# Optimization experiments

Hardware: AMD Instinct MI355X
Metric: run time of the kernel (lower is better)

Reference implementation:

```python
import jax, jax.numpy as jnp
import numpy as np

B, S, D = 4, 4096, 1024

def setup_inputs() -> dict:
    key = jax.random.key(0)
    ks = jax.random.split(key, 7)
    s = 1.0 / np.sqrt(D)
    return {
        "x":   jax.random.normal(ks[0], (B, S, D), dtype=jnp.float32),
        "Wq":  jax.random.uniform(ks[1], (D, D), jnp.float32, -s, s),
        "bq":  jax.random.uniform(ks[2], (D,),   jnp.float32, -s, s),
        "Wk":  jax.random.uniform(ks[3], (D, D), jnp.float32, -s, s),
        "bk":  jax.random.uniform(ks[4], (D,),   jnp.float32, -s, s),
        "Wv":  jax.random.uniform(ks[5], (D, D), jnp.float32, -s, s),
        "bv":  jax.random.uniform(ks[6], (D,),   jnp.float32, -s, s),
    }

def reference(x, Wq, bq, Wk, bk, Wv, bv):
    # Linear projections (torch Linear: x @ W.T + b; here W stored as [in, out])
    Q = jnp.einsum('bsd,df->bsf', x, Wq) + bq
    K = jnp.einsum('bsd,df->bsf', x, Wk) + bk
    V = jnp.einsum('bsd,df->bsf', x, Wv) + bv
    scale = 1.0 / jnp.sqrt(jnp.asarray(D, dtype=jnp.float32))
    scores = jnp.einsum('bqd,bkd->bqk', Q, K) * scale  # [B, S, S]
    attn = jax.nn.softmax(scores, axis=-1)
    return jnp.einsum('bqk,bkd->bqd', attn, V)
```

## Files before the change

kernel.cpp:

```cpp
#include <hip/hip_runtime.h>
#include <hip/hip_bf16.h>
#include <stdint.h>


typedef __attribute__((ext_vector_type(8))) short bf16x8;
typedef __attribute__((ext_vector_type(4))) float f32x4;

static __device__ __forceinline__ unsigned short f2b(float f) {
  union { float f; unsigned u; } x; x.f = f;
  unsigned u = x.u;
  u += 0x7fffu + ((u >> 16) & 1u);
  return (unsigned short)(u >> 16);
}
static __device__ __forceinline__ float b2f(unsigned short s) {
  union { unsigned u; float f; } x; x.u = ((unsigned)s) << 16;
  return x.f;
}

static __device__ __forceinline__ void gl_lds16(const void* g, void* l) {
  __builtin_amdgcn_global_load_lds(
      (const __attribute__((address_space(1))) void*)(uintptr_t)(g),
      (__attribute__((address_space(3))) void*)(uint32_t)(uintptr_t)(l),
      16, 0, 0);
}

__global__ void convert_x(const float* __restrict__ in,
                          unsigned short* __restrict__ out, int n8) {
  int i = blockIdx.x * blockDim.x + threadIdx.x;
  if (i >= n8) return;
  const float4* p = (const float4*)in + (size_t)i * 2;
  float4 a = p[0], b = p[1];
  bf16x8 o;
  o[0] = (short)f2b(a.x); o[1] = (short)f2b(a.y);
  o[2] = (short)f2b(a.z); o[3] = (short)f2b(a.w);
  o[4] = (short)f2b(b.x); o[5] = (short)f2b(b.y);
  o[6] = (short)f2b(b.z); o[7] = (short)f2b(b.w);
  ((bf16x8*)out)[i] = o;
}

__global__ void transpose_w(const float* __restrict__ in,
                            unsigned short* __restrict__ out) {
  __shared__ float tile[32][33];
  const int tx = threadIdx.x;
  const int x = blockIdx.x * 32 + tx;
  const int y0 = blockIdx.y * 32;
  for (int j = threadIdx.y; j < 32; j += 8)
    tile[j][tx] = in[(size_t)(y0 + j) * 1024 + x];
  __syncthreads();
  const int ox = blockIdx.y * 32 + tx;
  const int oy0 = blockIdx.x * 32;
  for (int j = threadIdx.y; j < 32; j += 8)
    out[(size_t)(oy0 + j) * 1024 + ox] = f2b(tile[tx][j]);
}

template <int OUTF>
__global__ __launch_bounds__(512, 2)
void gemm256(const unsigned short* __restrict__ A, long lda, long sAz,
             const unsigned short* __restrict__ B, long ldb, long sBz,
             void* __restrict__ Cv, long ldc, long sCz,
             const float* __restrict__ bias, int bias_mode,
             int K, float alpha) {
  __shared__ __align__(16) unsigned short As[2][256 * 64];
  __shared__ __align__(16) unsigned short Bs[2][256 * 64];

  const unsigned gx = gridDim.x, gy = gridDim.y;
  const unsigned nwg = gx * gy * gridDim.z;
  const unsigned hwid = (blockIdx.z * gy + blockIdx.y) * gx + blockIdx.x;
  unsigned tile = hwid;
  if ((nwg & 7u) == 0u) tile = (hwid & 7u) * (nwg >> 3) + (hwid >> 3);
  const unsigned bxi = tile % gx;
  const unsigned byi = (tile / gx) % gy;
  const unsigned bzi = tile / (gx * gy);

  const int t = threadIdx.x;
  const int wid = t >> 6, lane = t & 63;
  const int wm = wid >> 2, wn = wid & 3;
  const int fr = lane & 15, fq = lane >> 4;
  const long bm = (long)byi * 256;
  const long bn = (long)bxi * 256;
  const unsigned short* Ab = A + (size_t)bzi * sAz;
  const unsigned short* Bb = B + (size_t)bzi * sBz;

  const int sr = t >> 3;
  const int scol = 8 * ((t & 7) ^ (sr & 7));
  const unsigned short* Ag = Ab + (bm + sr) * lda + scol;
  const unsigned short* Bg = Bb + (bn + sr) * ldb + scol;
  const int ldsw = wid * 512;

  const int NT = K >> 6;
  f32x4 acc[8][4] = {};

#define STAGE(XS, Xg, ld, kt, h, bidx)                                        \
  do {                                                                        \
    gl_lds16(Xg + (size_t)((h) * 128) * (ld) + (size_t)(kt) * 64,             \
             &XS[bidx][(h) * 128 * 64 + ldsw]);                               \
    gl_lds16(Xg + (size_t)((h) * 128 + 64) * (ld) + (size_t)(kt) * 64,        \
             &XS[bidx][((h) * 128 + 64) * 64 + ldsw]);                        \
  } while (0)

  auto rdA = [&](int bidx, int i, int kh) {
    int row = wm * 128 + i * 16 + fr;
    int inb = (kh * 64 + fq * 16) ^ ((fr & 7) << 4);
    return *(const bf16x8*)((const char*)&As[bidx][0] + row * 128 + inb);
  };
  auto rdB = [&](int bidx, int j, int kh) {
    int row = wn * 64 + j * 16 + fr;
    int inb = (kh * 64 + fq * 16) ^ ((fr & 7) << 4);
    return *(const bf16x8*)((const char*)&Bs[bidx][0] + row * 128 + inb);
  };

  STAGE(As, Ag, lda, 0, 0, 0); STAGE(As, Ag, lda, 0, 1, 0);
  STAGE(Bs, Bg, ldb, 0, 0, 0); STAGE(Bs, Bg, ldb, 0, 1, 0);
  asm volatile("s_waitcnt vmcnt(0)" ::: "memory");
  asm volatile("s_barrier" ::: "memory");

  for (int tt = 0; tt < NT; ++tt) {
    const int bidx = tt & 1;
    const int nb = (tt + 1) & 1;
    bf16x8 bfr[4][2], ar[2][2], arn[2][2];

#pragma unroll
    for (int j = 0; j < 4; ++j) {
      bfr[j][0] = rdB(bidx, j, 0);
      bfr[j][1] = rdB(bidx, j, 1);
    }
#pragma unroll
    for (int ii = 0; ii < 2; ++ii) {
      ar[ii][0] = rdA(bidx, ii, 0);
      ar[ii][1] = rdA(bidx, ii, 1);
    }

    if (tt + 1 < NT) {
      STAGE(As, Ag, lda, tt + 1, 0, nb); STAGE(As, Ag, lda, tt + 1, 1, nb);
      STAGE(Bs, Bg, ldb, tt + 1, 0, nb); STAGE(Bs, Bg, ldb, tt + 1, 1, nb);
    }

    __builtin_amdgcn_s_setprio(1);
#pragma unroll
    for (int p = 0; p < 4; ++p) {
      if (p < 3) {
#pragma unroll
        for (int ii = 0; ii < 2; ++ii) {
          arn[ii][0] = rdA(bidx, (p + 1) * 2 + ii, 0);
          arn[ii][1] = rdA(bidx, (p + 1) * 2 + ii, 1);
        }
      }
#pragma unroll
      for (int ii = 0; ii < 2; ++ii)
#pragma unroll
        for (int j = 0; j < 4; ++j) {
          acc[p * 2 + ii][j] = __builtin_amdgcn_mfma_f32_16x16x32_bf16(
              ar[ii][0], bfr[j][0], acc[p * 2 + ii][j], 0, 0, 0);
          acc[p * 2 + ii][j] = __builtin_amdgcn_mfma_f32_16x16x32_bf16(
              ar[ii][1], bfr[j][1], acc[p * 2 + ii][j], 0, 0, 0);
        }
      if (p < 3) {
#pragma unroll
        for (int ii = 0; ii < 2; ++ii) {
          ar[ii][0] = arn[ii][0];
          ar[ii][1] = arn[ii][1];
        }
      }
    }
    __builtin_amdgcn_s_setprio(0);

    asm volatile("s_waitcnt vmcnt(0)" ::: "memory");
    asm volatile("s_barrier" ::: "memory");
  }
#undef STAGE

  char* Cb = (char*)Cv + (size_t)bzi * sCz * (OUTF ? 4 : 2);
  const long crow0 = bm + wm * 128 + fq * 4;
  const long ccol0 = bn + wn * 64 + fr;
#pragma unroll
  for (int i = 0; i < 8; ++i) {
#pragma unroll
    for (int j = 0; j < 4; ++j) {
      const long col = ccol0 + j * 16;
      float badd_c = (bias_mode == 1) ? bias[col] : 0.0f;
#pragma unroll
      for (int r = 0; r < 4; ++r) {
        const long row = crow0 + i * 16 + r;
        float v = acc[i][j][r] * alpha + badd_c;
        if (bias_mode == 2) v += bias[row];
        if (OUTF)
          ((float*)Cb)[row * ldc + col] = v;
        else
          ((unsigned short*)Cb)[row * ldc + col] = f2b(v);
      }
    }
  }
}

__global__ __launch_bounds__(256)
void softmax_rows(unsigned short* __restrict__ S) {
  const int t = threadIdx.x;
  unsigned short* row = S + (size_t)blockIdx.x * 4096;
  const bf16x8* p = (const bf16x8*)row;
  bf16x8 u0 = p[t * 2], u1 = p[t * 2 + 1];

  float v[16];
  float m = -1e30f;
#pragma unroll
  for (int j = 0; j < 8; j++) { v[j] = b2f((unsigned short)u0[j]); }
#pragma unroll
  for (int j = 0; j < 8; j++) { v[8 + j] = b2f((unsigned short)u1[j]); }
#pragma unroll
  for (int j = 0; j < 16; j++) m = fmaxf(m, v[j]);

#pragma unroll
  for (int off = 32; off > 0; off >>= 1) m = fmaxf(m, __shfl_xor(m, off));
  __shared__ float redm[4];
  if ((t & 63) == 0) redm[t >> 6] = m;
  __syncthreads();
  m = fmaxf(fmaxf(redm[0], redm[1]), fmaxf(redm[2], redm[3]));

  float s = 0.0f;
#pragma unroll
  for (int j = 0; j < 16; j++) { v[j] = __expf(v[j] - m); s += v[j]; }
#pragma unroll
  for (int off = 32; off > 0; off >>= 1) s += __shfl_xor(s, off);
  __shared__ float reds[4];
  if ((t & 63) == 0) reds[t >> 6] = s;
  __syncthreads();
  s = reds[0] + reds[1] + reds[2] + reds[3];
  const float inv = 1.0f / s;

  bf16x8 o0, o1;
#pragma unroll
  for (int j = 0; j < 8; j++) o0[j] = (short)f2b(v[j] * inv);
#pragma unroll
  for (int j = 0; j < 8; j++) o1[j] = (short)f2b(v[8 + j] * inv);
  bf16x8* q = (bf16x8*)row;
  q[t * 2] = o0;
  q[t * 2 + 1] = o1;
}

extern "C" void kernel_launch(void* const* d_in, const int* in_sizes, int n_in,
                              void* d_out, int out_size, void* d_ws,
                              size_t ws_size, hipStream_t stream) {
  const float* x  = (const float*)d_in[0];
  const float* Wq = (const float*)d_in[1];
  const float* bq = (const float*)d_in[2];
  const float* Wk = (const float*)d_in[3];
  const float* bk = (const float*)d_in[4];
  const float* Wv = (const float*)d_in[5];
  const float* bv = (const float*)d_in[6];
  float* out = (float*)d_out;

  const int Bb = 4, S = 4096, D = 1024;
  const long BS = (long)Bb * S;
  const size_t MiB = 1u << 20;

  char* base = (char*)d_ws;
  unsigned short* Wqt = (unsigned short*)(base);
  unsigned short* Wkt = (unsigned short*)(base + 2 * MiB);
  unsigned short* Wvt = (unsigned short*)(base + 4 * MiB);
  unsigned short* Qb  = (unsigned short*)(base + 6 * MiB);
  unsigned short* Kb  = (unsigned short*)(base + 38 * MiB);
  unsigned short* Vt  = (unsigned short*)(base + 70 * MiB);
  unsigned short* xb  = (unsigned short*)(base + 102 * MiB);
  unsigned short* Sb  = xb;
  const bool batched = ws_size >= (size_t)(102 + 128) * MiB;

  const int n8 = (int)(BS * D / 8);
  convert_x<<<n8 / 256, 256, 0, stream>>>(x, xb, n8);

  dim3 tb(32, 8), tg(32, 32);
  transpose_w<<<tg, tb, 0, stream>>>(Wq, Wqt);
  transpose_w<<<tg, tb, 0, stream>>>(Wk, Wkt);
  transpose_w<<<tg, tb, 0, stream>>>(Wv, Wvt);

  gemm256<0><<<dim3(D / 256, BS / 256, 1), 512, 0, stream>>>(
      xb, D, 0, Wqt, D, 0, Qb, D, 0, bq, 1, D, 1.0f);
  gemm256<0><<<dim3(D / 256, BS / 256, 1), 512, 0, stream>>>(
      xb, D, 0, Wkt, D, 0, Kb, D, 0, bk, 1, D, 1.0f);
  gemm256<0><<<dim3(BS / 256, D / 256, 1), 512, 0, stream>>>(
      Wvt, D, 0, xb, D, 0, Vt, BS, 0, bv, 2, D, 1.0f);

  const float scale = 0.03125f;
  if (batched) {
    gemm256<0><<<dim3(S / 256, S / 256, Bb), 512, 0, stream>>>(
        Qb, D, (long)S * D, Kb, D, (long)S * D, Sb, S, (long)S * S,
        nullptr, 0, D, scale);
    softmax_rows<<<Bb * S, 256, 0, stream>>>(Sb);
    gemm256<1><<<dim3(D / 256, S / 256, Bb), 512, 0, stream>>>(
        Sb, S, (long)S * S, Vt, BS, (long)S, out, D, (long)S * D,
        nullptr, 0, S, 1.0f);
  } else {
    for (int b = 0; b < Bb; b++) {
      const unsigned short* Qp = Qb + (long)b * S * D;
      const unsigned short* Kp = Kb + (long)b * S * D;
      gemm256<0><<<dim3(S / 256, S / 256, 1), 512, 0, stream>>>(
          Qp, D, 0, Kp, D, 0, Sb, S, 0, nullptr, 0, D, scale);
      softmax_rows<<<S, 256, 0, stream>>>(Sb);
      gemm256<1><<<dim3(D / 256, S / 256, 1), 512, 0, stream>>>(
          Sb, S, 0, Vt + (long)b * S, BS, 0, out + (long)b * S * D, D, 0,
          nullptr, 0, S, 1.0f);
    }
  }
}
```

Measured before the change: 463.9 us.

## Split GEMM K-tile into two half-phases with finer-grained async staging

Reorganizes shared-memory tiles into per-K-half sub-buffers (32 columns each) with a new XOR swizzle. The main loop now runs two phases per 64-wide K tile, each issuing that half's next-tile loads before its MFMAs and waiting only on partial vmcnt. This lets loads and compute interleave at a finer granularity instead of waiting on all loads at the end of each tile. The cost is an extra barrier per tile and more complex vmcnt bookkeeping, where a miscount could cause a race.

```diff
diff --git a/kernel.cpp b/kernel.cpp
--- a/kernel.cpp
+++ b/kernel.cpp
@@ -60,8 +60,8 @@
              void* __restrict__ Cv, long ldc, long sCz,
              const float* __restrict__ bias, int bias_mode,
              int K, float alpha) {
-  __shared__ __align__(16) unsigned short As[2][256 * 64];
-  __shared__ __align__(16) unsigned short Bs[2][256 * 64];
+  __shared__ __align__(16) unsigned short As[2][2][8192];
+  __shared__ __align__(16) unsigned short Bs[2][2][8192];
 
   const unsigned gx = gridDim.x, gy = gridDim.y;
   const unsigned nwg = gx * gy * gridDim.z;
@@ -81,93 +81,80 @@
   const unsigned short* Ab = A + (size_t)bzi * sAz;
   const unsigned short* Bb = B + (size_t)bzi * sBz;
 
-  const int sr = t >> 3;
-  const int scol = 8 * ((t & 7) ^ (sr & 7));
-  const unsigned short* Ag = Ab + (bm + sr) * lda + scol;
-  const unsigned short* Bg = Bb + (bn + sr) * ldb + scol;
-  const int ldsw = wid * 512;
+  const int srow = t >> 2;
+  const int soct8 = (((t & 3) ^ ((t >> 3) & 3))) * 8;
+  const unsigned short* AgS = Ab + (bm + srow) * lda + soct8;
+  const unsigned short* BgS = Bb + (bn + srow) * ldb + soct8;
+  const int dstw = wid * 512;
+  const int rs16 = (fq ^ ((fr >> 1) & 3)) << 4;
 
   const int NT = K >> 6;
   f32x4 acc[8][4] = {};
 
-#define STAGE(XS, Xg, ld, kt, h, bidx)                                        \
+  auto stg = [&](const unsigned short* GS, long ld, unsigned short* region,
+                 int kt, int kh) {
+    const unsigned short* s0 = GS + (size_t)kt * 64 + kh * 32;
+    gl_lds16(s0, region + dstw);
+    gl_lds16(s0 + (size_t)128 * ld, region + 4096 + dstw);
+  };
+  auto rdA = [&](int buf, int kh, int i) {
+    return *(const bf16x8*)((const char*)&As[buf][kh][0] +
+                            (wm * 128 + i * 16 + fr) * 64 + rs16);
+  };
+  auto rdB = [&](int buf, int kh, int j) {
+    return *(const bf16x8*)((const char*)&Bs[buf][kh][0] +
+                            (wn * 64 + j * 16 + fr) * 64 + rs16);
+  };
+
+  stg(AgS, lda, &As[0][0][0], 0, 0); stg(BgS, ldb, &Bs[0][0][0], 0, 0);
+  stg(AgS, lda, &As[0][1][0], 0, 1); stg(BgS, ldb, &Bs[0][1][0], 0, 1);
+  asm volatile("s_waitcnt vmcnt(4)" ::: "memory");
+  asm volatile("s_barrier" ::: "memory");
+
+#define PHASE(kh)                                                             \
   do {                                                                        \
-    gl_lds16(Xg + (size_t)((h) * 128) * (ld) + (size_t)(kt) * 64,             \
-             &XS[bidx][(h) * 128 * 64 + ldsw]);                               \
-    gl_lds16(Xg + (size_t)((h) * 128 + 64) * (ld) + (size_t)(kt) * 64,        \
-             &XS[bidx][((h) * 128 + 64) * 64 + ldsw]);                        \
+    if (tt + 1 < NT) {                                                        \
+      stg(AgS, lda, &As[nb][kh][0], tt + 1, kh);                              \
+      stg(BgS, ldb, &Bs[nb][kh][0], tt + 1, kh);                              \
+    }                                                                         \
+    bf16x8 bfr[4], ar[2], arn[2];                                             \
+    _Pragma("unroll")                                                         \
+    for (int j = 0; j < 4; ++j) bfr[j] = rdB(cb, kh, j);                      \
+    ar[0] = rdA(cb, kh, 0); ar[1] = rdA(cb, kh, 1);                           \
+    __builtin_amdgcn_s_setprio(1);                                            \
+    _Pragma("unroll")                                                         \
+    for (int p = 0; p < 4; ++p) {                                             \
+      if (p < 3) {                                                            \
+        arn[0] = rdA(cb, kh, p * 2 + 2);                                      \
+        arn[1] = rdA(cb, kh, p * 2 + 3);                                      \
+      }                                                                       \
+      _Pragma("unroll")                                                       \
+      for (int ii = 0; ii < 2; ++ii)                                          \
+        _Pragma("unroll")                                                     \
+        for (int j = 0; j < 4; ++j)                                           \
+          acc[p * 2 + ii][j] = __builtin_amdgcn_mfma_f32_16x16x32_bf16(       \
+              ar[ii], bfr[j], acc[p * 2 + ii][j], 0, 0, 0);                   \
+      if (p < 3) { ar[0] = arn[0]; ar[1] = arn[1]; }                          \
+    }                                                                         \
+    __builtin_amdgcn_s_setprio(0);                                            \
   } while (0)
 
-  auto rdA = [&](int bidx, int i, int kh) {
-    int row = wm * 128 + i * 16 + fr;
-    int inb = (kh * 64 + fq * 16) ^ ((fr & 7) << 4);
-    return *(const bf16x8*)((const char*)&As[bidx][0] + row * 128 + inb);
-  };
-  auto rdB = [&](int bidx, int j, int kh) {
-    int row = wn * 64 + j * 16 + fr;
-    int inb = (kh * 64 + fq * 16) ^ ((fr & 7) << 4);
-    return *(const bf16x8*)((const char*)&Bs[bidx][0] + row * 128 + inb);
-  };
-
-  STAGE(As, Ag, lda, 0, 0, 0); STAGE(As, Ag, lda, 0, 1, 0);
-  STAGE(Bs, Bg, ldb, 0, 0, 0); STAGE(Bs, Bg, ldb, 0, 1, 0);
-  asm volatile("s_waitcnt vmcnt(0)" ::: "memory");
-  asm volatile("s_barrier" ::: "memory");
-
   for (int tt = 0; tt < NT; ++tt) {
-    const int bidx = tt & 1;
-    const int nb = (tt + 1) & 1;
-    bf16x8 bfr[4][2], ar[2][2], arn[2][2];
-
-#pragma unroll
-    for (int j = 0; j < 4; ++j) {
-      bfr[j][0] = rdB(bidx, j, 0);
-      bfr[j][1] = rdB(bidx, j, 1);
-    }
-#pragma unroll
-    for (int ii = 0; ii < 2; ++ii) {
-      ar[ii][0] = rdA(bidx, ii, 0);
-      ar[ii][1] = rdA(bidx, ii, 1);
-    }
-
+    const int cb = tt & 1, nb = (tt + 1) & 1;
+    if (tt > 0) {
+      asm volatile("s_waitcnt vmcnt(4)" ::: "memory");
+      asm volatile("s_barrier" ::: "memory");
+    }
+    PHASE(0);
     if (tt + 1 < NT) {
-      STAGE(As, Ag, lda, tt + 1, 0, nb); STAGE(As, Ag, lda, tt + 1, 1, nb);
-      STAGE(Bs, Bg, ldb, tt + 1, 0, nb); STAGE(Bs, Bg, ldb, tt + 1, 1, nb);
-    }
-
-    __builtin_amdgcn_s_setprio(1);
-#pragma unroll
-    for (int p = 0; p < 4; ++p) {
-      if (p < 3) {
-#pragma unroll
-        for (int ii = 0; ii < 2; ++ii) {
-          arn[ii][0] = rdA(bidx, (p + 1) * 2 + ii, 0);
-          arn[ii][1] = rdA(bidx, (p + 1) * 2 + ii, 1);
-        }
-      }
-#pragma unroll
-      for (int ii = 0; ii < 2; ++ii)
-#pragma unroll
-        for (int j = 0; j < 4; ++j) {
-          acc[p * 2 + ii][j] = __builtin_amdgcn_mfma_f32_16x16x32_bf16(
-              ar[ii][0], bfr[j][0], acc[p * 2 + ii][j], 0, 0, 0);
-          acc[p * 2 + ii][j] = __builtin_amdgcn_mfma_f32_16x16x32_bf16(
-              ar[ii][1], bfr[j][1], acc[p * 2 + ii][j], 0, 0, 0);
-        }
-      if (p < 3) {
-#pragma unroll
-        for (int ii = 0; ii < 2; ++ii) {
-          ar[ii][0] = arn[ii][0];
-          ar[ii][1] = arn[ii][1];
-        }
-      }
-    }
-    __builtin_amdgcn_s_setprio(0);
-
-    asm volatile("s_waitcnt vmcnt(0)" ::: "memory");
+      asm volatile("s_waitcnt vmcnt(4)" ::: "memory");
+    } else {
+      asm volatile("s_waitcnt vmcnt(0)" ::: "memory");
+    }
     asm volatile("s_barrier" ::: "memory");
+    PHASE(1);
   }
-#undef STAGE
+#undef PHASE
 
   char* Cb = (char*)Cv + (size_t)bzi * sCz * (OUTF ? 4 : 2);
   const long crow0 = bm + wm * 128 + fq * 4;
```

Measured after the change: 483.5 us. 4.2% more time.

## Switch GEMM to 32x32x16 MFMA with 4 waves per 256x256 tile

Applied to the files above, without the earlier changes.

The GEMM kernel moves from 8 waves issuing 16x16x32 bf16 MFMAs to 4 waves (256 threads) each computing a 128x128 sub-tile with 32x32x16 MFMAs. Each wave reuses more of its LDS fragments per load, so fewer LDS reads are needed per FLOP. The global-to-LDS prefetch of the next tile is now issued before the current tile's fragments are read. In exchange, each lane holds 256 accumulator floats, which raises register pressure. With only 4 waves per block and dropped occupancy hints, there is less latency hiding, and the epilogue store pattern changes.

```diff
diff --git a/kernel.cpp b/kernel.cpp
--- a/kernel.cpp
+++ b/kernel.cpp
@@ -4,7 +4,7 @@
 
 
 typedef __attribute__((ext_vector_type(8))) short bf16x8;
-typedef __attribute__((ext_vector_type(4))) float f32x4;
+typedef __attribute__((ext_vector_type(16))) float f32x16;
 
 static __device__ __forceinline__ unsigned short f2b(float f) {
   union { float f; unsigned u; } x; x.f = f;
@@ -54,7 +54,7 @@
 }
 
 template <int OUTF>
-__global__ __launch_bounds__(512, 2)
+__global__ __launch_bounds__(256)
 void gemm256(const unsigned short* __restrict__ A, long lda, long sAz,
              const unsigned short* __restrict__ B, long ldb, long sBz,
              void* __restrict__ Cv, long ldc, long sCz,
@@ -74,92 +74,77 @@
 
   const int t = threadIdx.x;
   const int wid = t >> 6, lane = t & 63;
-  const int wm = wid >> 2, wn = wid & 3;
-  const int fr = lane & 15, fq = lane >> 4;
+  const int wm = wid >> 1, wn = wid & 1;
+  const int fr = lane & 31;
+  const int fh = lane >> 5;
   const long bm = (long)byi * 256;
   const long bn = (long)bxi * 256;
   const unsigned short* Ab = A + (size_t)bzi * sAz;
   const unsigned short* Bb = B + (size_t)bzi * sBz;
 
-  const int sr = t >> 3;
-  const int scol = 8 * ((t & 7) ^ (sr & 7));
-  const unsigned short* Ag = Ab + (bm + sr) * lda + scol;
-  const unsigned short* Bg = Bb + (bn + sr) * ldb + scol;
-  const int ldsw = wid * 512;
+  const int srow = t >> 3;
+  const int scol = 8 * ((t & 7) ^ ((t >> 3) & 7));
+  const unsigned short* AgS = Ab + (bm + srow) * lda + scol;
+  const unsigned short* BgS = Bb + (bn + srow) * ldb + scol;
+  const int dstw = wid * 512;
 
   const int NT = K >> 6;
-  f32x4 acc[8][4] = {};
-
-#define STAGE(XS, Xg, ld, kt, h, bidx)                                        \
-  do {                                                                        \
-    gl_lds16(Xg + (size_t)((h) * 128) * (ld) + (size_t)(kt) * 64,             \
-             &XS[bidx][(h) * 128 * 64 + ldsw]);                               \
-    gl_lds16(Xg + (size_t)((h) * 128 + 64) * (ld) + (size_t)(kt) * 64,        \
-             &XS[bidx][((h) * 128 + 64) * 64 + ldsw]);                        \
-  } while (0)
-
-  auto rdA = [&](int bidx, int i, int kh) {
-    int row = wm * 128 + i * 16 + fr;
-    int inb = (kh * 64 + fq * 16) ^ ((fr & 7) << 4);
-    return *(const bf16x8*)((const char*)&As[bidx][0] + row * 128 + inb);
+  f32x16 acc[4][4] = {};
+
+  auto stage_tile = [&](int kt, int buf) {
+#pragma unroll
+    for (int h = 0; h < 8; ++h)
+      gl_lds16(AgS + (size_t)(h * 32) * lda + (size_t)kt * 64,
+               &As[buf][h * 2048 + dstw]);
+#pragma unroll
+    for (int h = 0; h < 8; ++h)
+      gl_lds16(BgS + (size_t)(h * 32) * ldb + (size_t)kt * 64,
+               &Bs[buf][h * 2048 + dstw]);
   };
-  auto rdB = [&](int bidx, int j, int kh) {
-    int row = wn * 64 + j * 16 + fr;
-    int inb = (kh * 64 + fq * 16) ^ ((fr & 7) << 4);
-    return *(const bf16x8*)((const char*)&Bs[bidx][0] + row * 128 + inb);
+
+  auto rdA = [&](int buf, int i, int ks) {
+    const int row = wm * 128 + i * 32 + fr;
+    const int sl = ((ks * 2 + fh) ^ (row & 7)) << 4;
+    return *(const bf16x8*)((const char*)&As[buf][0] + row * 128 + sl);
   };
-
-  STAGE(As, Ag, lda, 0, 0, 0); STAGE(As, Ag, lda, 0, 1, 0);
-  STAGE(Bs, Bg, ldb, 0, 0, 0); STAGE(Bs, Bg, ldb, 0, 1, 0);
+  auto rdB = [&](int buf, int j, int ks) {
+    const int row = wn * 128 + j * 32 + fr;
+    const int sl = ((ks * 2 + fh) ^ (row & 7)) << 4;
+    return *(const bf16x8*)((const char*)&Bs[buf][0] + row * 128 + sl);
+  };
+
+  stage_tile(0, 0);
   asm volatile("s_waitcnt vmcnt(0)" ::: "memory");
   asm volatile("s_barrier" ::: "memory");
 
   for (int tt = 0; tt < NT; ++tt) {
-    const int bidx = tt & 1;
-    const int nb = (tt + 1) & 1;
-    bf16x8 bfr[4][2], ar[2][2], arn[2][2];
-
-#pragma unroll
-    for (int j = 0; j < 4; ++j) {
-      bfr[j][0] = rdB(bidx, j, 0);
-      bfr[j][1] = rdB(bidx, j, 1);
-    }
-#pragma unroll
-    for (int ii = 0; ii < 2; ++ii) {
-      ar[ii][0] = rdA(bidx, ii, 0);
-      ar[ii][1] = rdA(bidx, ii, 1);
-    }
-
-    if (tt + 1 < NT) {
-      STAGE(As, Ag, lda, tt + 1, 0, nb); STAGE(As, Ag, lda, tt + 1, 1, nb);
-      STAGE(Bs, Bg, ldb, tt + 1, 0, nb); STAGE(Bs, Bg, ldb, tt + 1, 1, nb);
-    }
+    const int cb = tt & 1, nb = (tt + 1) & 1;
+    if (tt + 1 < NT) stage_tile(tt + 1, nb);
+
+    bf16x8 a[4], b[4], an[4], bn[4];
+#pragma unroll
+    for (int i = 0; i < 4; ++i) a[i] = rdA(cb, i, 0);
+#pragma unroll
+    for (int j = 0; j < 4; ++j) b[j] = rdB(cb, j, 0);
 
     __builtin_amdgcn_s_setprio(1);
 #pragma unroll
-    for (int p = 0; p < 4; ++p) {
-      if (p < 3) {
-#pragma unroll
-        for (int ii = 0; ii < 2; ++ii) {
-          arn[ii][0] = rdA(bidx, (p + 1) * 2 + ii, 0);
-          arn[ii][1] = rdA(bidx, (p + 1) * 2 + ii, 1);
-        }
+    for (int ks = 0; ks < 4; ++ks) {
+      if (ks < 3) {
+#pragma unroll
+        for (int i = 0; i < 4; ++i) an[i] = rdA(cb, i, ks + 1);
+#pragma unroll
+        for (int j = 0; j < 4; ++j) bn[j] = rdB(cb, j, ks + 1);
       }
 #pragma unroll
-      for (int ii = 0; ii < 2; ++ii)
-#pragma unroll
-        for (int j = 0; j < 4; ++j) {
-          acc[p * 2 + ii][j] = __builtin_amdgcn_mfma_f32_16x16x32_bf16(
-              ar[ii][0], bfr[j][0], acc[p * 2 + ii][j], 0, 0, 0);
-          acc[p * 2 + ii][j] = __builtin_amdgcn_mfma_f32_16x16x32_bf16(
-              ar[ii][1], bfr[j][1], acc[p * 2 + ii][j], 0, 0, 0);
-        }
-      if (p < 3) {
-#pragma unroll
-        for (int ii = 0; ii < 2; ++ii) {
-          ar[ii][0] = arn[ii][0];
-          ar[ii][1] = arn[ii][1];
-        }
+      for (int i = 0; i < 4; ++i)
+#pragma unroll
+        for (int j = 0; j < 4; ++j)
+          acc[i][j] = __builtin_amdgcn_mfma_f32_32x32x16_bf16(
+              a[i], b[j], acc[i][j], 0, 0, 0);
+      if (ks < 3) {
+#pragma unroll
+        for (int i = 0; i < 4; ++i) { a[i] = an[i]; b[i] = bn[i]; }
       }
     }
     __builtin_amdgcn_s_setprio(0);
@@ -167,20 +152,19 @@
     asm volatile("s_waitcnt vmcnt(0)" ::: "memory");
     asm volatile("s_barrier" ::: "memory");
   }
-#undef STAGE
 
   char* Cb = (char*)Cv + (size_t)bzi * sCz * (OUTF ? 4 : 2);
-  const long crow0 = bm + wm * 128 + fq * 4;
-  const long ccol0 = bn + wn * 64 + fr;
-#pragma unroll
-  for (int i = 0; i < 8; ++i) {
+  const long crow0 = bm + wm * 128;
+  const long ccol0 = bn + wn * 128;
+#pragma unroll
+  for (int i = 0; i < 4; ++i) {
 #pragma unroll
     for (int j = 0; j < 4; ++j) {
-      const long col = ccol0 + j * 16;
+      const long col = ccol0 + j * 32 + fr;
       float badd_c = (bias_mode == 1) ? bias[col] : 0.0f;
 #pragma unroll
-      for (int r = 0; r < 4; ++r) {
-        const long row = crow0 + i * 16 + r;
+      for (int r = 0; r < 16; ++r) {
+        const long row = crow0 + i * 32 + (r & 3) + 8 * (r >> 2) + 4 * fh;
         float v = acc[i][j][r] * alpha + badd_c;
         if (bias_mode == 2) v += bias[row];
         if (OUTF)
@@ -271,30 +255,30 @@
   transpose_w<<<tg, tb, 0, stream>>>(Wk, Wkt);
   transpose_w<<<tg, tb, 0, stream>>>(Wv, Wvt);
 
-  gemm256<0><<<dim3(D / 256, BS / 256, 1), 512, 0, stream>>>(
+  gemm256<0><<<dim3(D / 256, BS / 256, 1), 256, 0, stream>>>(
       xb, D, 0, Wqt, D, 0, Qb, D, 0, bq, 1, D, 1.0f);
-  gemm256<0><<<dim3(D / 256, BS / 256, 1), 512, 0, stream>>>(
+  gemm256<0><<<dim3(D / 256, BS / 256, 1), 256, 0, stream>>>(
       xb, D, 0, Wkt, D, 0, Kb, D, 0, bk, 1, D, 1.0f);
-  gemm256<0><<<dim3(BS / 256, D / 256, 1), 512, 0, stream>>>(
+  gemm256<0><<<dim3(BS / 256, D / 256, 1), 256, 0, stream>>>(
       Wvt, D, 0, xb, D, 0, Vt, BS, 0, bv, 2, D, 1.0f);
 
   const float scale = 0.03125f;
   if (batched) {
-    gemm256<0><<<dim3(S / 256, S / 256, Bb), 512, 0, stream>>>(
+    gemm256<0><<<dim3(S / 256, S / 256, Bb), 256, 0, stream>>>(
         Qb, D, (long)S * D, Kb, D, (long)S * D, Sb, S, (long)S * S,
         nullptr, 0, D, scale);
     softmax_rows<<<Bb * S, 256, 0, stream>>>(Sb);
-    gemm256<1><<<dim3(D / 256, S / 256, Bb), 512, 0, stream>>>(
+    gemm256<1><<<dim3(D / 256, S / 256, Bb), 256, 0, stream>>>(
         Sb, S, (long)S * S, Vt, BS, (long)S, out, D, (long)S * D,
         nullptr, 0, S, 1.0f);
   } else {
     for (int b = 0; b < Bb; b++) {
       const unsigned short* Qp = Qb + (long)b * S * D;
       const unsigned short* Kp = Kb + (long)b * S * D;
-      gemm256<0><<<dim3(S / 256, S / 256, 1), 512, 0, stream>>>(
+      gemm256<0><<<dim3(S / 256, S / 256, 1), 256, 0, stream>>>(
           Qp, D, 0, Kp, D, 0, Sb, S, 0, nullptr, 0, D, scale);
       softmax_rows<<<S, 256, 0, stream>>>(Sb);
-      gemm256<1><<<dim3(D / 256, S / 256, 1), 512, 0, stream>>>(
+      gemm256<1><<<dim3(D / 256, S / 256, 1), 256, 0, stream>>>(
           Sb, S, 0, Vt + (long)b * S, BS, 0, out + (long)b * S * D, D, 0,
           nullptr, 0, S, 1.0f);
     }
```

After: 532.8 us. 1.15x slower.

## Shrink GEMM tiles to 128x128 and fuse Q/K projections into one GEMM

Applied to the files above, without the earlier changes.

The 256x256, 512-thread GEMM is replaced by a 128x128, 256-thread variant with four waves that each compute a 64x64 sub-tile. Wq and Wk are transposed into one concatenated weight so that Q and K come from a single GEMM writing an interleaved [BS, 2048] buffer, with the bias chosen per column by a split index. The smaller tiles are meant to give more workgroups and better occupancy and wave balance on the GPU. The cost is less data reuse per tile, so more global and LDS traffic per FLOP.

```diff
diff --git a/kernel.cpp b/kernel.cpp
--- a/kernel.cpp
+++ b/kernel.cpp
@@ -54,14 +54,14 @@
 }
 
 template <int OUTF>
-__global__ __launch_bounds__(512, 2)
-void gemm256(const unsigned short* __restrict__ A, long lda, long sAz,
+__global__ __launch_bounds__(256, 2)
+void gemm128(const unsigned short* __restrict__ A, long lda, long sAz,
              const unsigned short* __restrict__ B, long ldb, long sBz,
              void* __restrict__ Cv, long ldc, long sCz,
-             const float* __restrict__ bias, int bias_mode,
-             int K, float alpha) {
-  __shared__ __align__(16) unsigned short As[2][256 * 64];
-  __shared__ __align__(16) unsigned short Bs[2][256 * 64];
+             const float* __restrict__ ba, const float* __restrict__ bb,
+             int nsplit, int bias_mode, int K, float alpha) {
+  __shared__ __align__(16) unsigned short As[2][128 * 64];
+  __shared__ __align__(16) unsigned short Bs[2][128 * 64];
 
   const unsigned gx = gridDim.x, gy = gridDim.y;
   const unsigned nwg = gx * gy * gridDim.z;
@@ -74,75 +74,73 @@
 
   const int t = threadIdx.x;
   const int wid = t >> 6, lane = t & 63;
-  const int wm = wid >> 2, wn = wid & 3;
+  const int wm = wid >> 1, wn = wid & 1;
   const int fr = lane & 15, fq = lane >> 4;
-  const long bm = (long)byi * 256;
-  const long bn = (long)bxi * 256;
+  const long bm = (long)byi * 128;
+  const long bn = (long)bxi * 128;
   const unsigned short* Ab = A + (size_t)bzi * sAz;
   const unsigned short* Bb = B + (size_t)bzi * sBz;
 
   const int sr = t >> 3;
   const int scol = 8 * ((t & 7) ^ (sr & 7));
-  const unsigned short* Ag = Ab + (bm + sr) * lda + scol;
-  const unsigned short* Bg = Bb + (bn + sr) * ldb + scol;
+  const unsigned short* AgS = Ab + (bm + sr) * lda + scol;
+  const unsigned short* BgS = Bb + (bn + sr) * ldb + scol;
   const int ldsw = wid * 512;
 
   const int NT = K >> 6;
-  f32x4 acc[8][4] = {};
-
-#define STAGE(XS, Xg, ld, kt, h, bidx)                                        \
-  do {                                                                        \
-    gl_lds16(Xg + (size_t)((h) * 128) * (ld) + (size_t)(kt) * 64,             \
-             &XS[bidx][(h) * 128 * 64 + ldsw]);                               \
-    gl_lds16(Xg + (size_t)((h) * 128 + 64) * (ld) + (size_t)(kt) * 64,        \
-             &XS[bidx][((h) * 128 + 64) * 64 + ldsw]);                        \
-  } while (0)
-
-  auto rdA = [&](int bidx, int i, int kh) {
-    int row = wm * 128 + i * 16 + fr;
-    int inb = (kh * 64 + fq * 16) ^ ((fr & 7) << 4);
-    return *(const bf16x8*)((const char*)&As[bidx][0] + row * 128 + inb);
+  f32x4 acc[4][4] = {};
+
+  auto stage_tile = [&](int kt, int buf) {
+#pragma unroll
+    for (int h = 0; h < 4; ++h)
+      gl_lds16(AgS + (size_t)(h * 32) * lda + (size_t)kt * 64,
+               &As[buf][h * 2048 + ldsw]);
+#pragma unroll
+    for (int h = 0; h < 4; ++h)
+      gl_lds16(BgS + (size_t)(h * 32) * ldb + (size_t)kt * 64,
+               &Bs[buf][h * 2048 + ldsw]);
   };
-  auto rdB = [&](int bidx, int j, int kh) {
-    int row = wn * 64 + j * 16 + fr;
-    int inb = (kh * 64 + fq * 16) ^ ((fr & 7) << 4);
-    return *(const bf16x8*)((const char*)&Bs[bidx][0] + row * 128 + inb);
+
+  auto rdA = [&](int buf, int m, int kh) {
+    const int row = wm * 64 + m * 16 + fr;
+    const int inb = (kh * 64 + fq * 16) ^ ((fr & 7) << 4);
+    return *(const bf16x8*)((const char*)&As[buf][0] + row * 128 + inb);
   };
-
-  STAGE(As, Ag, lda, 0, 0, 0); STAGE(As, Ag, lda, 0, 1, 0);
-  STAGE(Bs, Bg, ldb, 0, 0, 0); STAGE(Bs, Bg, ldb, 0, 1, 0);
+  auto rdB = [&](int buf, int j, int kh) {
+    const int row = wn * 64 + j * 16 + fr;
+    const int inb = (kh * 64 + fq * 16) ^ ((fr & 7) << 4);
+    return *(const bf16x8*)((const char*)&Bs[buf][0] + row * 128 + inb);
+  };
+
+  stage_tile(0, 0);
   asm volatile("s_waitcnt vmcnt(0)" ::: "memory");
   asm volatile("s_barrier" ::: "memory");
 
   for (int tt = 0; tt < NT; ++tt) {
-    const int bidx = tt & 1;
-    const int nb = (tt + 1) & 1;
+    const int cb = tt & 1, nb = (tt + 1) & 1;
     bf16x8 bfr[4][2], ar[2][2], arn[2][2];
 
 #pragma unroll
     for (int j = 0; j < 4; ++j) {
-      bfr[j][0] = rdB(bidx, j, 0);
-      bfr[j][1] = rdB(bidx, j, 1);
+      bfr[j][0] = rdB(cb, j, 0);
+      bfr[j][1] = rdB(cb, j, 1);
     }
 #pragma unroll
     for (int ii = 0; ii < 2; ++ii) {
-      ar[ii][0] = rdA(bidx, ii, 0);
-      ar[ii][1] = rdA(bidx, ii, 1);
-    }
-
-    if (tt + 1 < NT) {
-      STAGE(As, Ag, lda, tt + 1, 0, nb); STAGE(As, Ag, lda, tt + 1, 1, nb);
-      STAGE(Bs, Bg, ldb, tt + 1, 0, nb); STAGE(Bs, Bg, ldb, tt + 1, 1, nb);
-    }
+      ar[ii][0] = rdA(cb, ii, 0);
+      ar[ii][1] = rdA(cb, ii, 1);
+    }
+
+    if (tt + 1 < NT) stage_tile(tt + 1, nb);
 
     __builtin_amdgcn_s_setprio(1);
 #pragma unroll
-    for (int p = 0; p < 4; ++p) {
-      if (p < 3) {
+    for (int p = 0; p < 2; ++p) {
+      if (p < 1) {
 #pragma unroll
         for (int ii = 0; ii < 2; ++ii) {
-          arn[ii][0] = rdA(bidx, (p + 1) * 2 + ii, 0);
-          arn[ii][1] = rdA(bidx, (p + 1) * 2 + ii, 1);
+          arn[ii][0] = rdA(cb, 2 + ii, 0);
+          arn[ii][1] = rdA(cb, 2 + ii, 1);
         }
       }
 #pragma unroll
@@ -154,7 +152,7 @@
           acc[p * 2 + ii][j] = __builtin_amdgcn_mfma_f32_16x16x32_bf16(
               ar[ii][1], bfr[j][1], acc[p * 2 + ii][j], 0, 0, 0);
         }
-      if (p < 3) {
+      if (p < 1) {
 #pragma unroll
         for (int ii = 0; ii < 2; ++ii) {
           ar[ii][0] = arn[ii][0];
@@ -167,22 +165,23 @@
     asm volatile("s_waitcnt vmcnt(0)" ::: "memory");
     asm volatile("s_barrier" ::: "memory");
   }
-#undef STAGE
 
   char* Cb = (char*)Cv + (size_t)bzi * sCz * (OUTF ? 4 : 2);
-  const long crow0 = bm + wm * 128 + fq * 4;
+  const long crow0 = bm + wm * 64 + fq * 4;
   const long ccol0 = bn + wn * 64 + fr;
 #pragma unroll
-  for (int i = 0; i < 8; ++i) {
+  for (int i = 0; i < 4; ++i) {
 #pragma unroll
     for (int j = 0; j < 4; ++j) {
       const long col = ccol0 + j * 16;
-      float badd_c = (bias_mode == 1) ? bias[col] : 0.0f;
+      float badd_c = 0.0f;
+      if (bias_mode == 1)
+        badd_c = (col < nsplit) ? ba[col] : bb[col - nsplit];
 #pragma unroll
       for (int r = 0; r < 4; ++r) {
         const long row = crow0 + i * 16 + r;
         float v = acc[i][j][r] * alpha + badd_c;
-        if (bias_mode == 2) v += bias[row];
+        if (bias_mode == 2) v += ba[row];
         if (OUTF)
           ((float*)Cb)[row * ldc + col] = v;
         else
@@ -253,50 +252,47 @@
   const size_t MiB = 1u << 20;
 
   char* base = (char*)d_ws;
-  unsigned short* Wqt = (unsigned short*)(base);
-  unsigned short* Wkt = (unsigned short*)(base + 2 * MiB);
-  unsigned short* Wvt = (unsigned short*)(base + 4 * MiB);
-  unsigned short* Qb  = (unsigned short*)(base + 6 * MiB);
-  unsigned short* Kb  = (unsigned short*)(base + 38 * MiB);
-  unsigned short* Vt  = (unsigned short*)(base + 70 * MiB);
-  unsigned short* xb  = (unsigned short*)(base + 102 * MiB);
-  unsigned short* Sb  = xb;
+  unsigned short* Wqkt = (unsigned short*)(base);
+  unsigned short* Wvt  = (unsigned short*)(base + 4 * MiB);
+  unsigned short* QK   = (unsigned short*)(base + 6 * MiB);
+  unsigned short* Vt   = (unsigned short*)(base + 70 * MiB);
+  unsigned short* xb   = (unsigned short*)(base + 102 * MiB);
+  unsigned short* Sb   = xb;
   const bool batched = ws_size >= (size_t)(102 + 128) * MiB;
 
   const int n8 = (int)(BS * D / 8);
   convert_x<<<n8 / 256, 256, 0, stream>>>(x, xb, n8);
 
   dim3 tb(32, 8), tg(32, 32);
-  transpose_w<<<tg, tb, 0, stream>>>(Wq, Wqt);
-  transpose_w<<<tg, tb, 0, stream>>>(Wk, Wkt);
+  transpose_w<<<tg, tb, 0, stream>>>(Wq, Wqkt);
+  transpose_w<<<tg, tb, 0, stream>>>(Wk, Wqkt + (size_t)D * D);
   transpose_w<<<tg, tb, 0, stream>>>(Wv, Wvt);
 
-  gemm256<0><<<dim3(D / 256, BS / 256, 1), 512, 0, stream>>>(
-      xb, D, 0, Wqt, D, 0, Qb, D, 0, bq, 1, D, 1.0f);
-  gemm256<0><<<dim3(D / 256, BS / 256, 1), 512, 0, stream>>>(
-      xb, D, 0, Wkt, D, 0, Kb, D, 0, bk, 1, D, 1.0f);
-  gemm256<0><<<dim3(BS / 256, D / 256, 1), 512, 0, stream>>>(
-      Wvt, D, 0, xb, D, 0, Vt, BS, 0, bv, 2, D, 1.0f);
-
+  gemm128<0><<<dim3(2048 / 128, BS / 128, 1), 256, 0, stream>>>(
+      xb, D, 0, Wqkt, D, 0, QK, 2048, 0, bq, bk, D, 1, D, 1.0f);
+  gemm128<0><<<dim3(BS / 128, D / 128, 1), 256, 0, stream>>>(
+      Wvt, D, 0, xb, D, 0, Vt, BS, 0, bv, nullptr, 0, 2, D, 1.0f);
+
+  const unsigned short* Qp = QK;
+  const unsigned short* Kp = QK + 1024;
   const float scale = 0.03125f;
   if (batched) {
-    gemm256<0><<<dim3(S / 256, S / 256, Bb), 512, 0, stream>>>(
-        Qb, D, (long)S * D, Kb, D, (long)S * D, Sb, S, (long)S * S,
-        nullptr, 0, D, scale);
+    gemm128<0><<<dim3(S / 128, S / 128, Bb), 256, 0, stream>>>(
+        Qp, 2048, (long)S * 2048, Kp, 2048, (long)S * 2048, Sb, S,
+        (long)S * S, nullptr, nullptr, 0, 0, D, scale);
     softmax_rows<<<Bb * S, 256, 0, stream>>>(Sb);
-    gemm256<1><<<dim3(D / 256, S / 256, Bb), 512, 0, stream>>>(
+    gemm128<1><<<dim3(D / 128, S / 128, Bb), 256, 0, stream>>>(
         Sb, S, (long)S * S, Vt, BS, (long)S, out, D, (long)S * D,
-        nullptr, 0, S, 1.0f);
+        nullptr, nullptr, 0, 0, S, 1.0f);
   } else {
     for (int b = 0; b < Bb; b++) {
-      const unsigned short* Qp = Qb + (long)b * S * D;
-      const unsigned short* Kp = Kb + (long)b * S * D;
-      gemm256<0><<<dim3(S / 256, S / 256, 1), 512, 0, stream>>>(
-          Qp, D, 0, Kp, D, 0, Sb, S, 0, nullptr, 0, D, scale);
+      gemm128<0><<<dim3(S / 128, S / 128, 1), 256, 0, stream>>>(
+          Qp + (long)b * S * 2048, 2048, 0, Kp + (long)b * S * 2048, 2048, 0,
+          Sb, S, 0, nullptr, nullptr, 0, 0, D, scale);
       softmax_rows<<<S, 256, 0, stream>>>(Sb);
-      gemm256<1><<<dim3(D / 256, S / 256, 1), 512, 0, stream>>>(
+      gemm128<1><<<dim3(D / 128, S / 128, 1), 256, 0, stream>>>(
           Sb, S, 0, Vt + (long)b * S, BS, 0, out + (long)b * S * D, D, 0,
-          nullptr, 0, S, 1.0f);
+          nullptr, nullptr, 0, 0, S, 1.0f);
     }
   }
 }
```

After: 514.9 us. 1.11x slower.
